# Performance work log

Measured on AMD Instinct MI355X. Metric: run time of the kernel, lower is better.

The kernel has to match this reference:

```python
import jax, jax.numpy as jnp
import numpy as np

N_HEADS = 16
NEG_INF = -1e30


def setup_inputs() -> dict:
    key = jax.random.key(0)
    ks = jax.random.split(key, 5)
    B, S, D = 2, 2048, 2048
    scale_w = 1.0 / np.sqrt(D)  # keep activations well-scaled
    return {
        "x": jax.random.normal(ks[0], (B, S, D), dtype=jnp.float32),
        "Wq": jax.random.normal(ks[1], (D, D), dtype=jnp.float32) * scale_w,
        "Wk": jax.random.normal(ks[2], (D, D), dtype=jnp.float32) * scale_w,
        "Wv": jax.random.normal(ks[3], (D, D), dtype=jnp.float32) * scale_w,
        "Wo": jax.random.normal(ks[4], (D, D), dtype=jnp.float32) * scale_w,
    }


def reference(x, Wq, Wk, Wv, Wo):
    # Blocked flash attention with online softmax is exactly causal softmax
    # attention; express it directly.
    B, S, D = x.shape
    H = N_HEADS
    dk = D // H
    scale = 1.0 / np.sqrt(dk)

    def heads(w):
        return (x @ w).reshape(B, S, H, dk)

    q = heads(Wq)  # [B,S,H,dk]
    k = heads(Wk)
    v = heads(Wv)

    scores = jnp.einsum("bqhd,bkhd->bhqk", q, k) * scale  # [B,H,S,S]
    causal = jnp.tril(jnp.ones((S, S), dtype=bool))
    scores = jnp.where(causal, scores, NEG_INF)
    p = jax.nn.softmax(scores, axis=-1)
    o = jnp.einsum("bhqk,bkhd->bqhd", p, v).reshape(B, S, D)
    return o @ Wo
```

## Files before the change

kernel.cpp:

```cpp
#include <hip/hip_runtime.h>
#include <hip/hip_bf16.h>

typedef short s16x8 __attribute__((ext_vector_type(8)));
typedef float f32x4 __attribute__((ext_vector_type(4)));
typedef unsigned short u16x4 __attribute__((ext_vector_type(4)));

#define MFMA16(a, b, c) __builtin_amdgcn_mfma_f32_16x16x32_bf16((a), (b), (c), 0, 0, 0)

__device__ __forceinline__ unsigned short f32_to_bf16(float f) {
  unsigned int u = __builtin_bit_cast(unsigned int, f);
  u += 0x7FFFu + ((u >> 16) & 1u);
  return (unsigned short)(u >> 16);
}

__device__ __forceinline__ void glds16(const unsigned short* g, unsigned short* l) {
  __builtin_amdgcn_global_load_lds(
      (const __attribute__((address_space(1))) void*)g,
      (__attribute__((address_space(3))) void*)l, 16, 0, 0);
}

__global__ void cvt_bf16_k(const float* __restrict__ in, unsigned short* __restrict__ out, int n4) {
  int i = blockIdx.x * 256 + threadIdx.x;
  if (i >= n4) return;
  float4 f = ((const float4*)in)[i];
  u16x4 o;
  o.x = f32_to_bf16(f.x); o.y = f32_to_bf16(f.y);
  o.z = f32_to_bf16(f.z); o.w = f32_to_bf16(f.w);
  ((u16x4*)out)[i] = o;
}

__global__ void cvt_t4_k(const float* __restrict__ Wq, const float* __restrict__ Wk,
                         const float* __restrict__ Wv, const float* __restrict__ Wo,
                         unsigned short* __restrict__ outQKV, unsigned short* __restrict__ outO,
                         int D) {
  int z = blockIdx.z;
  const float* in = (z == 0) ? Wq : (z == 1) ? Wk : (z == 2) ? Wv : Wo;
  unsigned short* out = (z < 3) ? (outQKV + (size_t)z * D * D) : outO;
  __shared__ float tile[32][33];
  int tx = threadIdx.x;
  int nt = D >> 5;
  int bx = blockIdx.x % nt;
  int by = blockIdx.x / nt;
  int r = tx >> 3, c4 = (tx & 7) * 4;
  int k0 = by * 32, n0 = bx * 32;
  float4 f = *(const float4*)(in + (size_t)(k0 + r) * D + n0 + c4);
  tile[r][c4 + 0] = f.x; tile[r][c4 + 1] = f.y;
  tile[r][c4 + 2] = f.z; tile[r][c4 + 3] = f.w;
  __syncthreads();
  u16x4 o;
  o.x = f32_to_bf16(tile[c4 + 0][r]);
  o.y = f32_to_bf16(tile[c4 + 1][r]);
  o.z = f32_to_bf16(tile[c4 + 2][r]);
  o.w = f32_to_bf16(tile[c4 + 3][r]);
  *(u16x4*)(out + (size_t)(n0 + r) * D + k0 + c4) = o;
}

template <int OUTF32>
__global__ __launch_bounds__(512, 2) void gemm3(
    const unsigned short* __restrict__ A, const unsigned short* __restrict__ Bt,
    void* __restrict__ Cv, int M, int N, int K, int ldc) {
  __shared__ unsigned short As[3][256 * 64];
  __shared__ unsigned short Bs[3][128 * 64];
  int t = threadIdx.x, lane = t & 63, w = t >> 6;
  int r16 = lane & 15, kg = lane >> 4;
  int wm = w >> 1, wn = w & 1;
  int nbn = N >> 7;
  int bm = blockIdx.x / nbn, bn = blockIdx.x % nbn;
  const unsigned short* Ag = A + (size_t)bm * 256 * K;
  const unsigned short* Bg = Bt + (size_t)bn * 128 * K;

  const unsigned short* asrc[4];
  const unsigned short* bsrc[2];
  int aoff[4], boff[2];
#pragma unroll
  for (int i = 0; i < 4; ++i) {
    int c = i * 512 + t;
    int row = c >> 3, sl = c & 7;
    asrc[i] = Ag + (size_t)row * K + ((sl ^ (row & 7)) * 8);
    aoff[i] = (i * 512 + (t & ~63)) * 8;
  }
#pragma unroll
  for (int i = 0; i < 2; ++i) {
    int c = i * 512 + t;
    int row = c >> 3, sl = c & 7;
    bsrc[i] = Bg + (size_t)row * K + ((sl ^ (row & 7)) * 8);
    boff[i] = (i * 512 + (t & ~63)) * 8;
  }

  auto STAGE = [&](int bi, int kt2) {
    int k0 = kt2 * 64;
#pragma unroll
    for (int i = 0; i < 4; ++i) glds16(asrc[i] + k0, &As[bi][aoff[i]]);
#pragma unroll
    for (int i = 0; i < 2; ++i) glds16(bsrc[i] + k0, &Bs[bi][boff[i]]);
  };

  f32x4 acc[4][4] = {};
  int nt = K >> 6;
  STAGE(0, 0);
  if (nt > 1) STAGE(1, 1);
  int cur = 0;
  for (int kt = 0; kt < nt; ++kt) {
    if (kt + 1 < nt) {
      asm volatile("s_waitcnt vmcnt(6)" ::: "memory");
    } else {
      asm volatile("s_waitcnt vmcnt(0)" ::: "memory");
    }
    __builtin_amdgcn_s_barrier();
    asm volatile("" ::: "memory");
    if (kt + 2 < nt) {
      int s2 = cur + 2; if (s2 >= 3) s2 -= 3;
      STAGE(s2, kt + 2);
    }
    const unsigned short* Al = As[cur];
    s16x8 af[4][2], bfr[4][2];
#pragma unroll
    for (int mf = 0; mf < 4; ++mf) {
      int row = wm * 64 + mf * 16 + r16;
#pragma unroll
      for (int ks = 0; ks < 2; ++ks)
        af[mf][ks] = *(const s16x8*)&Al[row * 64 + (((ks * 4 + kg) ^ (row & 7)) * 8)];
    }
#pragma unroll
    for (int nf = 0; nf < 4; ++nf) {
      int row = wn * 64 + nf * 16 + r16;
#pragma unroll
      for (int ks = 0; ks < 2; ++ks)
        bfr[nf][ks] = *(const s16x8*)&Bs[cur][row * 64 + (((ks * 4 + kg) ^ (row & 7)) * 8)];
    }
    __builtin_amdgcn_s_setprio(1);
#pragma unroll
    for (int ks = 0; ks < 2; ++ks)
#pragma unroll
      for (int mf = 0; mf < 4; ++mf)
#pragma unroll
        for (int nf = 0; nf < 4; ++nf)
          acc[mf][nf] = MFMA16(af[mf][ks], bfr[nf][ks], acc[mf][nf]);
    __builtin_amdgcn_s_setprio(0);
    cur = (cur == 2) ? 0 : cur + 1;
  }
#pragma unroll
  for (int mf = 0; mf < 4; ++mf)
#pragma unroll
    for (int nf = 0; nf < 4; ++nf)
#pragma unroll
      for (int r = 0; r < 4; ++r) {
        int row = bm * 256 + wm * 64 + mf * 16 + kg * 4 + r;
        int col = bn * 128 + wn * 64 + nf * 16 + r16;
        if (OUTF32)
          ((float*)Cv)[(size_t)row * ldc + col] = acc[mf][nf][r];
        else
          ((unsigned short*)Cv)[(size_t)row * ldc + col] = f32_to_bf16(acc[mf][nf][r]);
      }
}

__global__ __launch_bounds__(256) void vtr_k(const unsigned short* __restrict__ V,
                                             unsigned short* __restrict__ Vt,
                                             int S, int ld) {
  __shared__ unsigned short T[32 * 128];
  int s0 = blockIdx.x * 32, h = blockIdx.y, b = blockIdx.z;
  int H = gridDim.y;
  int t = threadIdx.x;
  const unsigned short* src = V + (size_t)(b * S + s0) * ld + h * 128;
#pragma unroll
  for (int c = 0; c < 2; ++c) {
    int chunk = c * 256 + t;
    int row = chunk >> 4, slot = chunk & 15;
    glds16(src + (size_t)row * ld + slot * 8, &T[(c * 256 + (t & ~63)) * 8]);
  }
  __syncthreads();
  unsigned short* dst = Vt + ((size_t)(b * H + h) * (S >> 3) + (s0 >> 3)) * 1024;
#pragma unroll
  for (int c = 0; c < 2; ++c) {
    int oc = c * 256 + t;
    int sl = oc >> 7, d = oc & 127;
    s16x8 v;
#pragma unroll
    for (int j = 0; j < 8; ++j) v[j] = (short)T[(sl * 8 + j) * 128 + d];
    *(s16x8*)(dst + (size_t)oc * 8) = v;
  }
}

__global__ __launch_bounds__(512) void attn2_k(
    const unsigned short* __restrict__ Q, const unsigned short* __restrict__ Kx,
    const unsigned short* __restrict__ Vt, unsigned short* __restrict__ O,
    int S, int D, int Bn, int ld) {
  const float scale = 0.08838834764831843f;
  int hb = blockIdx.x;
  int h = hb / Bn, b = hb % Bn;
  int NQ = S >> 7;
  int qt = NQ - 1 - blockIdx.y;
  int H = D >> 7;
  int t = threadIdx.x, lane = t & 63, w = t >> 6;
  int r16 = lane & 15, kg = lane >> 4;
  const unsigned short* Qb  = Q + (size_t)b * S * ld + h * 128;
  const unsigned short* Kb  = Kx + (size_t)b * S * ld + h * 128;
  const unsigned short* Vtb = Vt + (size_t)(b * H + h) * (S >> 3) * 1024;

  __shared__ unsigned short Kbuf[2][64 * 128];
  __shared__ unsigned short Vbuf[2][64 * 128];
  __shared__ unsigned short Pl[8][16 * 64];

  auto STAGE = [&](int bufi, int kv0) {
    const unsigned short* Ksrc = Kb + (size_t)kv0 * ld;
#pragma unroll
    for (int c = 0; c < 2; ++c) {
      int chunk = c * 512 + t;
      int row = chunk >> 4, slot = chunk & 15;
      glds16(Ksrc + (size_t)row * ld + ((slot ^ (row & 7)) * 8),
             &Kbuf[bufi][(c * 512 + (t & ~63)) * 8]);
    }
    const unsigned short* Vsrc = Vtb + (size_t)(kv0 >> 3) * 1024;
#pragma unroll
    for (int c = 0; c < 2; ++c) {
      int chunk = c * 512 + t;
      glds16(Vsrc + (size_t)chunk * 8, &Vbuf[bufi][(c * 512 + (t & ~63)) * 8]);
    }
  };

  int W0 = qt * 128 + w * 16;
  int qg = W0 + r16;
  s16x8 qf[4];
#pragma unroll
  for (int ks = 0; ks < 4; ++ks)
    qf[ks] = *(const s16x8*)(Qb + (size_t)qg * ld + ks * 32 + kg * 8);
  f32x4 oacc[8] = {};
  float m_st = -1e30f, l_st = 0.f;
  int nt = (qt + 1) * 2;
  int cur = 0;
  STAGE(0, 0);
  __syncthreads();
  for (int it = 0; it < nt; ++it) {
    int kv0 = it * 64;
    if (it + 1 < nt) STAGE(cur ^ 1, (it + 1) * 64);
    const unsigned short* Kl = Kbuf[cur];
    const unsigned short* Vl = Vbuf[cur];
    if (kv0 <= W0 + 15) {
      f32x4 st4[4];
      __builtin_amdgcn_s_setprio(1);
#pragma unroll
      for (int kf = 0; kf < 4; ++kf) {
        f32x4 s = {};
#pragma unroll
        for (int ks = 0; ks < 4; ++ks) {
          int row = kf * 16 + r16;
          s16x8 kfr = *(const s16x8*)&Kl[row * 128 + (((ks * 4 + kg) ^ (row & 7)) * 8)];
          s = MFMA16(kfr, qf[ks], s);
        }
        st4[kf] = s;
      }
      __builtin_amdgcn_s_setprio(0);
      float p[4][4];
      float mx = -1e30f;
#pragma unroll
      for (int kf = 0; kf < 4; ++kf)
#pragma unroll
        for (int r = 0; r < 4; ++r) {
          int kvg = kv0 + kf * 16 + kg * 4 + r;
          float sv = st4[kf][r] * scale;
          sv = (kvg <= qg) ? sv : -1e30f;
          p[kf][r] = sv;
          mx = fmaxf(mx, sv);
        }
      mx = fmaxf(mx, __shfl_xor(mx, 16, 64));
      mx = fmaxf(mx, __shfl_xor(mx, 32, 64));
      float m_new = fmaxf(m_st, mx);
      float alpha = __expf(m_st - m_new);
      float rs = 0.f;
#pragma unroll
      for (int kf = 0; kf < 4; ++kf)
#pragma unroll
        for (int r = 0; r < 4; ++r) {
          float e = __expf(p[kf][r] - m_new);
          p[kf][r] = e;
          rs += e;
        }
      rs += __shfl_xor(rs, 16, 64);
      rs += __shfl_xor(rs, 32, 64);
      l_st = l_st * alpha + rs;
      m_st = m_new;
#pragma unroll
      for (int kf = 0; kf < 4; ++kf) {
        unsigned int lo = (unsigned int)f32_to_bf16(p[kf][0]) | ((unsigned int)f32_to_bf16(p[kf][1]) << 16);
        unsigned int hi = (unsigned int)f32_to_bf16(p[kf][2]) | ((unsigned int)f32_to_bf16(p[kf][3]) << 16);
        int sslot = 2 * kf + (kg >> 1);
        int base = r16 * 64 + ((sslot ^ (r16 & 7)) * 8) + (kg & 1) * 4;
        *(unsigned int*)&Pl[w][base]     = lo;
        *(unsigned int*)&Pl[w][base + 2] = hi;
      }
      asm volatile("s_waitcnt lgkmcnt(0)" ::: "memory");
      __builtin_amdgcn_sched_barrier(0);
      float ar[4];
#pragma unroll
      for (int r = 0; r < 4; ++r) ar[r] = __shfl(alpha, kg * 4 + r, 64);
#pragma unroll
      for (int f = 0; f < 8; ++f)
#pragma unroll
        for (int r = 0; r < 4; ++r) oacc[f][r] *= ar[r];
      __builtin_amdgcn_s_setprio(1);
#pragma unroll
      for (int tt = 0; tt < 2; ++tt) {
        s16x8 pf = *(const s16x8*)&Pl[w][r16 * 64 + (((4 * tt + kg) ^ (r16 & 7)) * 8)];
#pragma unroll
        for (int f = 0; f < 8; ++f) {
          s16x8 vf = *(const s16x8*)&Vl[((4 * tt + kg) * 128 + f * 16 + r16) * 8];
          oacc[f] = MFMA16(pf, vf, oacc[f]);
        }
      }
      __builtin_amdgcn_s_setprio(0);
    }
    __syncthreads();
    cur ^= 1;
  }
  float linv = 1.0f / l_st;
  float lr[4];
#pragma unroll
  for (int r = 0; r < 4; ++r) lr[r] = __shfl(linv, kg * 4 + r, 64);
#pragma unroll
  for (int f = 0; f < 8; ++f)
#pragma unroll
    for (int r = 0; r < 4; ++r) {
      size_t idx = ((size_t)b * S + W0 + kg * 4 + r) * D + h * 128 + f * 16 + r16;
      O[idx] = f32_to_bf16(oacc[f][r] * lr[r]);
    }
}

extern "C" void kernel_launch(void* const* d_in, const int* in_sizes, int n_in,
                              void* d_out, int out_size, void* d_ws, size_t ws_size,
                              hipStream_t stream) {
  const float* x  = (const float*)d_in[0];
  const float* Wq = (const float*)d_in[1];
  const float* Wk = (const float*)d_in[2];
  const float* Wv = (const float*)d_in[3];
  const float* Wo = (const float*)d_in[4];
  const int D = 2048, H = 16;
  const int M = in_sizes[0] / D;
  const int B = 2, S = M / B;
  const int LD = 3 * D;

  unsigned short* xb    = (unsigned short*)d_ws;
  unsigned short* Wqkvt = xb + (size_t)M * D;
  unsigned short* Wot   = Wqkvt + (size_t)3 * D * D;
  unsigned short* QKVb  = Wot + (size_t)D * D;
  unsigned short* Ob    = xb;
  unsigned short* VtA   = Wqkvt;

  int n4 = M * D / 4;
  cvt_bf16_k<<<(n4 + 255) / 256, 256, 0, stream>>>(x, xb, n4);
  int tgrid = (D / 32) * (D / 32);
  cvt_t4_k<<<dim3(tgrid, 1, 4), 256, 0, stream>>>(Wq, Wk, Wv, Wo, Wqkvt, Wot, D);

  gemm3<0><<<(M / 256) * (LD / 128), 512, 0, stream>>>(xb, Wqkvt, QKVb, M, LD, D, LD);

  vtr_k<<<dim3(S / 32, H, B), 256, 0, stream>>>(QKVb + 2 * D, VtA, S, LD);

  attn2_k<<<dim3(H * B, S / 128), 512, 0, stream>>>(QKVb, QKVb + D, VtA, Ob, S, D, B, LD);

  gemm3<1><<<(M / 256) * (D / 128), 512, 0, stream>>>(Ob, Wot, d_out, M, D, D, D);
}
```

Before: 297.5 us.

## Add smaller-K-tile QKV GEMM variant and skip softmax rescale when max unchanged

```diff
diff --git a/kernel.cpp b/kernel.cpp
--- a/kernel.cpp
+++ b/kernel.cpp
@@ -56,6 +56,94 @@
 }
 
 template <int OUTF32>
+__global__ __launch_bounds__(512, 4) void gemm3b(
+    const unsigned short* __restrict__ A, const unsigned short* __restrict__ Bt,
+    void* __restrict__ Cv, int M, int N, int K, int ldc) {
+  __shared__ unsigned short As[3][256 * 32];
+  __shared__ unsigned short Bs[3][128 * 32];
+  int t = threadIdx.x, lane = t & 63, w = t >> 6;
+  int r16 = lane & 15, kg = lane >> 4;
+  int wm = w >> 1, wn = w & 1;
+  int nbn = N >> 7;
+  int bm = blockIdx.x / nbn, bn = blockIdx.x % nbn;
+  const unsigned short* Ag = A + (size_t)bm * 256 * K;
+  const unsigned short* Bg = Bt + (size_t)bn * 128 * K;
+
+  const unsigned short* asrc[2];
+  int aoff[2];
+#pragma unroll
+  for (int i = 0; i < 2; ++i) {
+    int c = i * 512 + t;
+    int row = c >> 2, sl = c & 3;
+    asrc[i] = Ag + (size_t)row * K + ((sl ^ (row & 3)) * 8);
+    aoff[i] = (i * 512 + (t & ~63)) * 8;
+  }
+  int brow = t >> 2;
+  const unsigned short* bsrc = Bg + (size_t)brow * K + (((t & 3) ^ (brow & 3)) * 8);
+  int boff = (t & ~63) * 8;
+
+  auto STAGE = [&](int bi, int kt2) {
+    int k0 = kt2 * 32;
+    glds16(asrc[0] + k0, &As[bi][aoff[0]]);
+    glds16(asrc[1] + k0, &As[bi][aoff[1]]);
+    glds16(bsrc + k0, &Bs[bi][boff]);
+  };
+
+  f32x4 acc[4][4] = {};
+  int nt = K >> 5;
+  STAGE(0, 0);
+  if (nt > 1) STAGE(1, 1);
+  int cur = 0;
+  for (int kt = 0; kt < nt; ++kt) {
+    if (kt + 1 < nt) {
+      asm volatile("s_waitcnt vmcnt(3)" ::: "memory");
+    } else {
+      asm volatile("s_waitcnt vmcnt(0)" ::: "memory");
+    }
+    __builtin_amdgcn_s_barrier();
+    asm volatile("" ::: "memory");
+    if (kt + 2 < nt) {
+      int s2 = cur + 2; if (s2 >= 3) s2 -= 3;
+      STAGE(s2, kt + 2);
+    }
+    const unsigned short* Al = As[cur];
+    const unsigned short* Bl = Bs[cur];
+    s16x8 af[4], bfr[4];
+#pragma unroll
+    for (int mf = 0; mf < 4; ++mf) {
+      int row = wm * 64 + mf * 16 + r16;
+      af[mf] = *(const s16x8*)&Al[row * 32 + ((kg ^ (row & 3)) * 8)];
+    }
+#pragma unroll
+    for (int nf = 0; nf < 4; ++nf) {
+      int row = wn * 64 + nf * 16 + r16;
+      bfr[nf] = *(const s16x8*)&Bl[row * 32 + ((kg ^ (row & 3)) * 8)];
+    }
+    __builtin_amdgcn_s_setprio(1);
+#pragma unroll
+    for (int mf = 0; mf < 4; ++mf)
+#pragma unroll
+      for (int nf = 0; nf < 4; ++nf)
+        acc[mf][nf] = MFMA16(af[mf], bfr[nf], acc[mf][nf]);
+    __builtin_amdgcn_s_setprio(0);
+    cur = (cur == 2) ? 0 : cur + 1;
+  }
+#pragma unroll
+  for (int mf = 0; mf < 4; ++mf)
+#pragma unroll
+    for (int nf = 0; nf < 4; ++nf)
+#pragma unroll
+      for (int r = 0; r < 4; ++r) {
+        int row = bm * 256 + wm * 64 + mf * 16 + kg * 4 + r;
+        int col = bn * 128 + wn * 64 + nf * 16 + r16;
+        if (OUTF32)
+          ((float*)Cv)[(size_t)row * ldc + col] = acc[mf][nf][r];
+        else
+          ((unsigned short*)Cv)[(size_t)row * ldc + col] = f32_to_bf16(acc[mf][nf][r]);
+      }
+}
+
+template <int OUTF32>
 __global__ __launch_bounds__(512, 2) void gemm3(
     const unsigned short* __restrict__ A, const unsigned short* __restrict__ Bt,
     void* __restrict__ Cv, int M, int N, int K, int ldc) {
@@ -264,8 +352,8 @@
         }
       mx = fmaxf(mx, __shfl_xor(mx, 16, 64));
       mx = fmaxf(mx, __shfl_xor(mx, 32, 64));
-      float m_new = fmaxf(m_st, mx);
-      float alpha = __expf(m_st - m_new);
+      bool skip = __all(mx <= m_st);
+      float m_new = skip ? m_st : fmaxf(m_st, mx);
       float rs = 0.f;
 #pragma unroll
       for (int kf = 0; kf < 4; ++kf)
@@ -277,8 +365,6 @@
         }
       rs += __shfl_xor(rs, 16, 64);
       rs += __shfl_xor(rs, 32, 64);
-      l_st = l_st * alpha + rs;
-      m_st = m_new;
 #pragma unroll
       for (int kf = 0; kf < 4; ++kf) {
         unsigned int lo = (unsigned int)f32_to_bf16(p[kf][0]) | ((unsigned int)f32_to_bf16(p[kf][1]) << 16);
@@ -290,13 +376,20 @@
       }
       asm volatile("s_waitcnt lgkmcnt(0)" ::: "memory");
       __builtin_amdgcn_sched_barrier(0);
-      float ar[4];
-#pragma unroll
-      for (int r = 0; r < 4; ++r) ar[r] = __shfl(alpha, kg * 4 + r, 64);
-#pragma unroll
-      for (int f = 0; f < 8; ++f)
-#pragma unroll
-        for (int r = 0; r < 4; ++r) oacc[f][r] *= ar[r];
+      if (!skip) {
+        float alpha = __expf(m_st - m_new);
+        l_st = l_st * alpha + rs;
+        m_st = m_new;
+        float ar[4];
+#pragma unroll
+        for (int r = 0; r < 4; ++r) ar[r] = __shfl(alpha, kg * 4 + r, 64);
+#pragma unroll
+        for (int f = 0; f < 8; ++f)
+#pragma unroll
+          for (int r = 0; r < 4; ++r) oacc[f][r] *= ar[r];
+      } else {
+        l_st += rs;
+      }
       __builtin_amdgcn_s_setprio(1);
 #pragma unroll
       for (int tt = 0; tt < 2; ++tt) {
@@ -350,7 +443,7 @@
   int tgrid = (D / 32) * (D / 32);
   cvt_t4_k<<<dim3(tgrid, 1, 4), 256, 0, stream>>>(Wq, Wk, Wv, Wo, Wqkvt, Wot, D);
 
-  gemm3<0><<<(M / 256) * (LD / 128), 512, 0, stream>>>(xb, Wqkvt, QKVb, M, LD, D, LD);
+  gemm3b<0><<<(M / 256) * (LD / 128), 512, 0, stream>>>(xb, Wqkvt, QKVb, M, LD, D, LD);
 
   vtr_k<<<dim3(S / 32, H, B), 256, 0, stream>>>(QKVb + 2 * D, VtA, S, LD);
 
```

Result: faster. 278.4 us (-6.4%).
